# Kernel optimization log

Hardware: AMD Instinct MI355X
Metric: run time of the kernel (lower is better)

Reference implementation:

```python
import jax, jax.numpy as jnp
import numpy as np

B = 8192            # batch.size
NNZ = B * 32        # active features per position ~32
FT = 512            # ft_out
F_FULL = 49152      # HalfKA feature count
F_VIRT = 768        # factorized (virtual) feature count


def setup_inputs() -> dict:
    key = jax.random.key(0)
    ks = jax.random.split(key, 8)
    s_ft = 1.0 / np.sqrt(F_FULL).astype(np.float32)
    s_fft = 1.0 / np.sqrt(F_VIRT).astype(np.float32)
    s_out = 1.0 / np.sqrt(2 * FT).astype(np.float32)
    return {
        "values": jnp.ones((NNZ,), dtype=jnp.float32),
        # W_ft stored feature-major [F_FULL, FT] = torch ft.weight.T, so rows are gathered per feature
        "W_ft": jax.random.uniform(ks[0], (F_FULL, FT), jnp.float32, -s_ft, s_ft),
        "ft_b": jax.random.uniform(ks[1], (FT,), jnp.float32, -s_ft, s_ft),
        "W_fft": jax.random.uniform(ks[2], (F_VIRT, FT), jnp.float32, -s_fft, s_fft),
        "fft_b": jax.random.uniform(ks[3], (FT,), jnp.float32, -s_fft, s_fft),
        "W_out": jax.random.uniform(ks[4], (1, 2 * FT), jnp.float32, -s_out, s_out),
        "out_b": jax.random.uniform(ks[5], (1,), jnp.float32, -s_out, s_out),
        "batch_ids": jnp.sort(jax.random.randint(ks[6], (NNZ,), 0, B)),
        "stm_feat": jax.random.randint(ks[7], (NNZ,), 0, F_FULL),
        "nstm_feat": jax.random.randint(jax.random.fold_in(key, 7), (NNZ,), 0, F_FULL),
        "size": B,
    }


def reference(values, W_ft, ft_b, W_fft, fft_b, W_out, out_b,
              batch_ids, stm_feat, nstm_feat, size):
    v = values[:, None]  # [NNZ, 1]

    def transform(feat):
        # sparse COO x dense weight == gather weight rows per active feature, scale, segment-sum
        acc = jax.ops.segment_sum(W_ft[feat] * v, batch_ids, num_segments=size)
        acc_v = jax.ops.segment_sum(W_fft[feat % F_VIRT] * v, batch_ids, num_segments=size)
        return acc + acc_v + ft_b + fft_b  # both Linear biases applied once per row

    stm_ft = transform(stm_feat)    # [B, FT]
    nstm_ft = transform(nstm_feat)  # [B, FT]
    hidden = jnp.clip(jnp.concatenate([stm_ft, nstm_ft], axis=1), 0.0, 1.0)
    return jax.nn.sigmoid(hidden @ W_out.T + out_b)  # [B, 1]
```

## Files before the change

kernel.cpp:

```cpp
#include <hip/hip_runtime.h>
#include <hip/hip_bf16.h>
#include <math.h>


constexpr int FT      = 512;
constexpr int FV      = 768;
constexpr int CHUNK   = 128;
constexpr int ROWS    = 4;

typedef __attribute__((ext_vector_type(8))) unsigned short ushort8_t;

__device__ inline unsigned short f2bf(float x) {
    union { float f; unsigned int u; } v; v.f = x;
    unsigned int r = v.u + 0x7FFFu + ((v.u >> 16) & 1u);
    return (unsigned short)(r >> 16);
}
__device__ inline float bf2f(unsigned short s) {
    union { unsigned int u; float f; } v; v.u = ((unsigned int)s) << 16;
    return v.f;
}

__global__ __launch_bounds__(256)
void prepass_kernel(const float* __restrict__ W_ft, const float* __restrict__ W_fft,
                    unsigned short* __restrict__ comb, int n8, int cgrid,
                    const int* __restrict__ batch_ids, int nnz, int B,
                    int* __restrict__ seg_start)
{
    if (blockIdx.x < (unsigned)cgrid) {
        int i = blockIdx.x * 256 + threadIdx.x;
        if (i >= n8) return;
        const int f    = i >> 6;
        const int base = i * 8;
        const int gcol = (i & 63) * 8;
        const int vrow = (f % FV) * FT + gcol;

        const float4 a0 = *(const float4*)(W_ft  + base);
        const float4 a1 = *(const float4*)(W_ft  + base + 4);
        const float4 b0 = *(const float4*)(W_fft + vrow);
        const float4 b1 = *(const float4*)(W_fft + vrow + 4);

        ushort8_t u;
        u[0] = f2bf(a0.x + b0.x); u[1] = f2bf(a0.y + b0.y);
        u[2] = f2bf(a0.z + b0.z); u[3] = f2bf(a0.w + b0.w);
        u[4] = f2bf(a1.x + b1.x); u[5] = f2bf(a1.y + b1.y);
        u[6] = f2bf(a1.z + b1.z); u[7] = f2bf(a1.w + b1.w);
        *(ushort8_t*)(comb + base) = u;
    } else {
        int b = (blockIdx.x - cgrid) * 256 + threadIdx.x;
        if (b > B) return;
        int lo = 0, hi = nnz;
        while (lo < hi) {
            int mid = (lo + hi) >> 1;
            if (batch_ids[mid] < b) lo = mid + 1; else hi = mid;
        }
        seg_start[b] = lo;
    }
}

__global__ __launch_bounds__(128)
void nnue_kernel(const float* __restrict__ values,
                 const unsigned short* __restrict__ Wc,
                 const float* __restrict__ ft_b,
                 const float* __restrict__ fft_b,
                 const float* __restrict__ W_out,
                 const float* __restrict__ out_b,
                 const int*   __restrict__ seg_start,
                 const int*   __restrict__ stm_feat,
                 const int*   __restrict__ nstm_feat,
                 float* __restrict__ out)
{
    const int t    = threadIdx.x;
    const int w    = t >> 6;
    const int lane = t & 63;
    const int col  = lane * 8;

    __shared__ int   sh_os[CHUNK];
    __shared__ int   sh_on[CHUNK];
    __shared__ float sh_v [CHUNK];
    __shared__ float sh_part[2][FT];

    for (int r = 0; r < ROWS; ++r) {
        const int b      = blockIdx.x * ROWS + r;
        const int seg_lo = seg_start[b];
        const int seg_hi = seg_start[b + 1];

        float acc_s[8] = {0,0,0,0,0,0,0,0};
        float acc_n[8] = {0,0,0,0,0,0,0,0};

        for (int base = seg_lo; base < seg_hi; base += CHUNK) {
            const int cnt = min(CHUNK, seg_hi - base);
            __syncthreads();
            if (t < cnt) {
                sh_os[t] = stm_feat [base + t] * FT;
                sh_on[t] = nstm_feat[base + t] * FT;
                sh_v [t] = values[base + t];
            }
            __syncthreads();

            #pragma unroll 4
            for (int j = w; j < cnt; j += 2) {
                const float v = sh_v[j];
                const ushort8_t a = *(const ushort8_t*)(Wc + sh_os[j] + col);
                const ushort8_t c = *(const ushort8_t*)(Wc + sh_on[j] + col);
                #pragma unroll
                for (int k = 0; k < 8; ++k) {
                    acc_s[k] = fmaf(bf2f(a[k]), v, acc_s[k]);
                    acc_n[k] = fmaf(bf2f(c[k]), v, acc_n[k]);
                }
            }
        }

        __syncthreads();
        if (w == 1) {
            #pragma unroll
            for (int k = 0; k < 8; ++k) {
                sh_part[0][col + k] = acc_s[k];
                sh_part[1][col + k] = acc_n[k];
            }
        }
        __syncthreads();

        if (w == 0) {
            #pragma unroll
            for (int k = 0; k < 8; ++k) {
                acc_s[k] += sh_part[0][col + k];
                acc_n[k] += sh_part[1][col + k];
            }

            const float4 fb0 = *(const float4*)(ft_b  + col);
            const float4 fb1 = *(const float4*)(ft_b  + col + 4);
            const float4 vb0 = *(const float4*)(fft_b + col);
            const float4 vb1 = *(const float4*)(fft_b + col + 4);
            const float4 ws0 = *(const float4*)(W_out + col);
            const float4 ws1 = *(const float4*)(W_out + col + 4);
            const float4 wn0 = *(const float4*)(W_out + FT + col);
            const float4 wn1 = *(const float4*)(W_out + FT + col + 4);

            const float bias[8] = { fb0.x + vb0.x, fb0.y + vb0.y, fb0.z + vb0.z, fb0.w + vb0.w,
                                    fb1.x + vb1.x, fb1.y + vb1.y, fb1.z + vb1.z, fb1.w + vb1.w };
            const float wos[8]  = { ws0.x, ws0.y, ws0.z, ws0.w, ws1.x, ws1.y, ws1.z, ws1.w };
            const float won[8]  = { wn0.x, wn0.y, wn0.z, wn0.w, wn1.x, wn1.y, wn1.z, wn1.w };

            float partial = 0.f;
            #pragma unroll
            for (int k = 0; k < 8; ++k) {
                float hs = fminf(fmaxf(acc_s[k] + bias[k], 0.f), 1.f);
                float hn = fminf(fmaxf(acc_n[k] + bias[k], 0.f), 1.f);
                partial = fmaf(hs, wos[k], partial);
                partial = fmaf(hn, won[k], partial);
            }

            #pragma unroll
            for (int off = 32; off > 0; off >>= 1)
                partial += __shfl_down(partial, off, 64);

            if (lane == 0)
                out[b] = 1.0f / (1.0f + expf(-(partial + out_b[0])));
        }
    }
}

__global__ __launch_bounds__(128)
void nnue_f32_kernel(const float* __restrict__ values,
                     const float* __restrict__ W_ft,
                     const float* __restrict__ ft_b,
                     const float* __restrict__ W_fft,
                     const float* __restrict__ fft_b,
                     const float* __restrict__ W_out,
                     const float* __restrict__ out_b,
                     const int*   __restrict__ batch_ids,
                     const int*   __restrict__ stm_feat,
                     const int*   __restrict__ nstm_feat,
                     int nnz,
                     float* __restrict__ out)
{
    const int b   = blockIdx.x;
    const int t   = threadIdx.x;
    const int col = t * 4;

    int lo0 = 0, hi0 = nnz;
    while (lo0 < hi0) {
        int mid = (lo0 + hi0) >> 1;
        if (batch_ids[mid] < b) lo0 = mid + 1; else hi0 = mid;
    }
    int lo1 = lo0, hi1 = nnz;
    while (lo1 < hi1) {
        int mid = (lo1 + hi1) >> 1;
        if (batch_ids[mid] < b + 1) lo1 = mid + 1; else hi1 = mid;
    }
    const int seg_lo = lo0, seg_hi = lo1;

    __shared__ int   sh_off_s [128];
    __shared__ int   sh_off_sv[128];
    __shared__ int   sh_off_n [128];
    __shared__ int   sh_off_nv[128];
    __shared__ float sh_v     [128];

    float4 acc_s = make_float4(0.f, 0.f, 0.f, 0.f);
    float4 acc_n = make_float4(0.f, 0.f, 0.f, 0.f);

    for (int base = seg_lo; base < seg_hi; base += 128) {
        const int cnt = min(128, seg_hi - base);
        __syncthreads();
        if (t < cnt) {
            int fs = stm_feat[base + t];
            int fn = nstm_feat[base + t];
            sh_off_s [t] = fs * FT;
            sh_off_sv[t] = (fs % FV) * FT;
            sh_off_n [t] = fn * FT;
            sh_off_nv[t] = (fn % FV) * FT;
            sh_v     [t] = values[base + t];
        }
        __syncthreads();

        #pragma unroll 2
        for (int j = 0; j < cnt; ++j) {
            const float v = sh_v[j];
            const float4 a  = *(const float4*)(W_ft  + sh_off_s [j] + col);
            const float4 av = *(const float4*)(W_fft + sh_off_sv[j] + col);
            const float4 c  = *(const float4*)(W_ft  + sh_off_n [j] + col);
            const float4 cv = *(const float4*)(W_fft + sh_off_nv[j] + col);
            acc_s.x = fmaf(a.x + av.x, v, acc_s.x);
            acc_s.y = fmaf(a.y + av.y, v, acc_s.y);
            acc_s.z = fmaf(a.z + av.z, v, acc_s.z);
            acc_s.w = fmaf(a.w + av.w, v, acc_s.w);
            acc_n.x = fmaf(c.x + cv.x, v, acc_n.x);
            acc_n.y = fmaf(c.y + cv.y, v, acc_n.y);
            acc_n.z = fmaf(c.z + cv.z, v, acc_n.z);
            acc_n.w = fmaf(c.w + cv.w, v, acc_n.w);
        }
    }

    const float4 fb  = *(const float4*)(ft_b  + col);
    const float4 vb  = *(const float4*)(fft_b + col);
    const float4 wos = *(const float4*)(W_out + col);
    const float4 won = *(const float4*)(W_out + FT + col);

    float partial = 0.f;
    {
        float h;
        h = fminf(fmaxf(acc_s.x + fb.x + vb.x, 0.f), 1.f); partial = fmaf(h, wos.x, partial);
        h = fminf(fmaxf(acc_s.y + fb.y + vb.y, 0.f), 1.f); partial = fmaf(h, wos.y, partial);
        h = fminf(fmaxf(acc_s.z + fb.z + vb.z, 0.f), 1.f); partial = fmaf(h, wos.z, partial);
        h = fminf(fmaxf(acc_s.w + fb.w + vb.w, 0.f), 1.f); partial = fmaf(h, wos.w, partial);
        h = fminf(fmaxf(acc_n.x + fb.x + vb.x, 0.f), 1.f); partial = fmaf(h, won.x, partial);
        h = fminf(fmaxf(acc_n.y + fb.y + vb.y, 0.f), 1.f); partial = fmaf(h, won.y, partial);
        h = fminf(fmaxf(acc_n.z + fb.z + vb.z, 0.f), 1.f); partial = fmaf(h, won.z, partial);
        h = fminf(fmaxf(acc_n.w + fb.w + vb.w, 0.f), 1.f); partial = fmaf(h, won.w, partial);
    }

    #pragma unroll
    for (int off = 32; off > 0; off >>= 1)
        partial += __shfl_down(partial, off, 64);

    __shared__ float wave_sum[2];
    if ((t & 63) == 0) wave_sum[t >> 6] = partial;
    __syncthreads();
    if (t == 0) {
        float s = wave_sum[0] + wave_sum[1] + out_b[0];
        out[b] = 1.0f / (1.0f + expf(-s));
    }
}

extern "C" void kernel_launch(void* const* d_in, const int* in_sizes, int n_in,
                              void* d_out, int out_size, void* d_ws, size_t ws_size,
                              hipStream_t stream) {
    const float* values    = (const float*)d_in[0];
    const float* W_ft      = (const float*)d_in[1];
    const float* ft_b      = (const float*)d_in[2];
    const float* W_fft     = (const float*)d_in[3];
    const float* fft_b     = (const float*)d_in[4];
    const float* W_out     = (const float*)d_in[5];
    const float* out_b     = (const float*)d_in[6];
    const int*   batch_ids = (const int*)d_in[7];
    const int*   stm_feat  = (const int*)d_in[8];
    const int*   nstm_feat = (const int*)d_in[9];

    const int nnz  = in_sizes[0];
    const int B    = out_size;
    const int n_ft = in_sizes[1];

    const size_t comb_bytes = (size_t)n_ft * sizeof(unsigned short);
    const size_t need = comb_bytes + (size_t)(B + 1) * sizeof(int);

    if (ws_size >= need && (B % ROWS) == 0) {
        unsigned short* comb = (unsigned short*)d_ws;
        int* seg_start = (int*)((char*)d_ws + comb_bytes);

        const int n8    = n_ft / 8;
        const int cgrid = (n8 + 255) / 256;
        const int bgrid = (B + 1 + 255) / 256;

        prepass_kernel<<<cgrid + bgrid, 256, 0, stream>>>(
            W_ft, W_fft, comb, n8, cgrid, batch_ids, nnz, B, seg_start);
        nnue_kernel<<<B / ROWS, 128, 0, stream>>>(
            values, comb, ft_b, fft_b, W_out, out_b,
            seg_start, stm_feat, nstm_feat, (float*)d_out);
    } else {
        nnue_f32_kernel<<<B, 128, 0, stream>>>(
            values, W_ft, ft_b, W_fft, fft_b, W_out, out_b,
            batch_ids, stm_feat, nstm_feat, nnz, (float*)d_out);
    }
}
```

Measured before the change: 215.9 us.

## Assign one wavefront per batch row and broadcast indices via readlane

Replaces the two-wave-per-row split, with its LDS staging and cross-wave reduction, by one 64-lane wavefront per batch row and four rows per 256-thread block. Feature offsets and values are loaded one per lane and broadcast with readlane, so there is no shared memory and no __syncthreads. This removes barrier and LDS overhead and lets rows run independently. In exchange each row's gather is serialized within a single wave, which lowers per-row memory-level parallelism.

```diff
diff --git a/kernel.cpp b/kernel.cpp
--- a/kernel.cpp
+++ b/kernel.cpp
@@ -1,12 +1,10 @@
 #include <hip/hip_runtime.h>
-#include <hip/hip_bf16.h>
 #include <math.h>
 
 
-constexpr int FT      = 512;
-constexpr int FV      = 768;
-constexpr int CHUNK   = 128;
-constexpr int ROWS    = 4;
+constexpr int FT    = 512;
+constexpr int FV    = 768;
+constexpr int ROWS  = 4;
 
 typedef __attribute__((ext_vector_type(8))) unsigned short ushort8_t;
 
@@ -57,7 +55,7 @@
     }
 }
 
-__global__ __launch_bounds__(128)
+__global__ __launch_bounds__(256, 4)
 void nnue_kernel(const float* __restrict__ values,
                  const unsigned short* __restrict__ Wc,
                  const float* __restrict__ ft_b,
@@ -67,97 +65,77 @@
                  const int*   __restrict__ seg_start,
                  const int*   __restrict__ stm_feat,
                  const int*   __restrict__ nstm_feat,
+                 int B,
                  float* __restrict__ out)
 {
-    const int t    = threadIdx.x;
-    const int w    = t >> 6;
-    const int lane = t & 63;
+    const int w    = threadIdx.x >> 6;
+    const int lane = threadIdx.x & 63;
     const int col  = lane * 8;
-
-    __shared__ int   sh_os[CHUNK];
-    __shared__ int   sh_on[CHUNK];
-    __shared__ float sh_v [CHUNK];
-    __shared__ float sh_part[2][FT];
-
-    for (int r = 0; r < ROWS; ++r) {
-        const int b      = blockIdx.x * ROWS + r;
-        const int seg_lo = seg_start[b];
-        const int seg_hi = seg_start[b + 1];
-
-        float acc_s[8] = {0,0,0,0,0,0,0,0};
-        float acc_n[8] = {0,0,0,0,0,0,0,0};
-
-        for (int base = seg_lo; base < seg_hi; base += CHUNK) {
-            const int cnt = min(CHUNK, seg_hi - base);
-            __syncthreads();
-            if (t < cnt) {
-                sh_os[t] = stm_feat [base + t] * FT;
-                sh_on[t] = nstm_feat[base + t] * FT;
-                sh_v [t] = values[base + t];
-            }
-            __syncthreads();
-
-            #pragma unroll 4
-            for (int j = w; j < cnt; j += 2) {
-                const float v = sh_v[j];
-                const ushort8_t a = *(const ushort8_t*)(Wc + sh_os[j] + col);
-                const ushort8_t c = *(const ushort8_t*)(Wc + sh_on[j] + col);
-                #pragma unroll
-                for (int k = 0; k < 8; ++k) {
-                    acc_s[k] = fmaf(bf2f(a[k]), v, acc_s[k]);
-                    acc_n[k] = fmaf(bf2f(c[k]), v, acc_n[k]);
-                }
-            }
-        }
-
-        __syncthreads();
-        if (w == 1) {
+    const int b    = blockIdx.x * ROWS + w;
+    if (b >= B) return;
+
+    const int seg_lo = seg_start[b];
+    const int seg_hi = seg_start[b + 1];
+
+    float acc_s[8] = {0,0,0,0,0,0,0,0};
+    float acc_n[8] = {0,0,0,0,0,0,0,0};
+
+    for (int base = seg_lo; base < seg_hi; base += 64) {
+        const int cnt = min(64, seg_hi - base);
+
+        int fso = 0, fno = 0; float val = 0.f;
+        if (lane < cnt) {
+            fso = stm_feat [base + lane] * FT;
+            fno = nstm_feat[base + lane] * FT;
+            val = values[base + lane];
+        }
+
+        #pragma unroll 4
+        for (int j = 0; j < cnt; ++j) {
+            const int   offs = __builtin_amdgcn_readlane(fso, j);
+            const int   offn = __builtin_amdgcn_readlane(fno, j);
+            const float v    = __int_as_float(
+                                 __builtin_amdgcn_readlane(__float_as_int(val), j));
+
+            const ushort8_t a = *(const ushort8_t*)(Wc + offs + col);
+            const ushort8_t c = *(const ushort8_t*)(Wc + offn + col);
             #pragma unroll
             for (int k = 0; k < 8; ++k) {
-                sh_part[0][col + k] = acc_s[k];
-                sh_part[1][col + k] = acc_n[k];
+                acc_s[k] = fmaf(bf2f(a[k]), v, acc_s[k]);
+                acc_n[k] = fmaf(bf2f(c[k]), v, acc_n[k]);
             }
         }
-        __syncthreads();
-
-        if (w == 0) {
-            #pragma unroll
-            for (int k = 0; k < 8; ++k) {
-                acc_s[k] += sh_part[0][col + k];
-                acc_n[k] += sh_part[1][col + k];
-            }
-
-            const float4 fb0 = *(const float4*)(ft_b  + col);
-            const float4 fb1 = *(const float4*)(ft_b  + col + 4);
-            const float4 vb0 = *(const float4*)(fft_b + col);
-            const float4 vb1 = *(const float4*)(fft_b + col + 4);
-            const float4 ws0 = *(const float4*)(W_out + col);
-            const float4 ws1 = *(const float4*)(W_out + col + 4);
-            const float4 wn0 = *(const float4*)(W_out + FT + col);
-            const float4 wn1 = *(const float4*)(W_out + FT + col + 4);
-
-            const float bias[8] = { fb0.x + vb0.x, fb0.y + vb0.y, fb0.z + vb0.z, fb0.w + vb0.w,
-                                    fb1.x + vb1.x, fb1.y + vb1.y, fb1.z + vb1.z, fb1.w + vb1.w };
-            const float wos[8]  = { ws0.x, ws0.y, ws0.z, ws0.w, ws1.x, ws1.y, ws1.z, ws1.w };
-            const float won[8]  = { wn0.x, wn0.y, wn0.z, wn0.w, wn1.x, wn1.y, wn1.z, wn1.w };
-
-            float partial = 0.f;
-            #pragma unroll
-            for (int k = 0; k < 8; ++k) {
-                float hs = fminf(fmaxf(acc_s[k] + bias[k], 0.f), 1.f);
-                float hn = fminf(fmaxf(acc_n[k] + bias[k], 0.f), 1.f);
-                partial = fmaf(hs, wos[k], partial);
-                partial = fmaf(hn, won[k], partial);
-            }
-
-            #pragma unroll
-            for (int off = 32; off > 0; off >>= 1)
-                partial += __shfl_down(partial, off, 64);
-
-            if (lane == 0)
-                out[b] = 1.0f / (1.0f + expf(-(partial + out_b[0])));
-        }
-    }
+    }
+
+    const float4 fb0 = *(const float4*)(ft_b  + col);
+    const float4 fb1 = *(const float4*)(ft_b  + col + 4);
+    const float4 vb0 = *(const float4*)(fft_b + col);
+    const float4 vb1 = *(const float4*)(fft_b + col + 4);
+    const float4 ws0 = *(const float4*)(W_out + col);
+    const float4 ws1 = *(const float4*)(W_out + col + 4);
+    const float4 wn0 = *(const float4*)(W_out + FT + col);
+    const float4 wn1 = *(const float4*)(W_out + FT + col + 4);
+
+    const float bias[8] = { fb0.x + vb0.x, fb0.y + vb0.y, fb0.z + vb0.z, fb0.w + vb0.w,
+                            fb1.x + vb1.x, fb1.y + vb1.y, fb1.z + vb1.z, fb1.w + vb1.w };
+    const float wos[8]  = { ws0.x, ws0.y, ws0.z, ws0.w, ws1.x, ws1.y, ws1.z, ws1.w };
+    const float won[8]  = { wn0.x, wn0.y, wn0.z, wn0.w, wn1.x, wn1.y, wn1.z, wn1.w };
+
+    float partial = 0.f;
+    #pragma unroll
+    for (int k = 0; k < 8; ++k) {
+        float hs = fminf(fmaxf(acc_s[k] + bias[k], 0.f), 1.f);
+        float hn = fminf(fmaxf(acc_n[k] + bias[k], 0.f), 1.f);
+        partial = fmaf(hs, wos[k], partial);
+        partial = fmaf(hn, won[k], partial);
+    }
+
+    #pragma unroll
+    for (int off = 32; off > 0; off >>= 1)
+        partial += __shfl_down(partial, off, 64);
+
+    if (lane == 0)
+        out[b] = 1.0f / (1.0f + expf(-(partial + out_b[0])));
 }
 
 __global__ __launch_bounds__(128)
@@ -283,7 +261,7 @@
     const size_t comb_bytes = (size_t)n_ft * sizeof(unsigned short);
     const size_t need = comb_bytes + (size_t)(B + 1) * sizeof(int);
 
-    if (ws_size >= need && (B % ROWS) == 0) {
+    if (ws_size >= need) {
         unsigned short* comb = (unsigned short*)d_ws;
         int* seg_start = (int*)((char*)d_ws + comb_bytes);
 
@@ -293,9 +271,9 @@
 
         prepass_kernel<<<cgrid + bgrid, 256, 0, stream>>>(
             W_ft, W_fft, comb, n8, cgrid, batch_ids, nnz, B, seg_start);
-        nnue_kernel<<<B / ROWS, 128, 0, stream>>>(
+        nnue_kernel<<<(B + ROWS - 1) / ROWS, 256, 0, stream>>>(
             values, comb, ft_b, fft_b, W_out, out_b,
-            seg_start, stm_feat, nstm_feat, (float*)d_out);
+            seg_start, stm_feat, nstm_feat, B, (float*)d_out);
     } else {
         nnue_f32_kernel<<<B, 128, 0, stream>>>(
             values, W_ft, ft_b, W_fft, fft_b, W_out, out_b,
```

New measurement: 217.0 us. Within noise of the previous version (+0.5%).
